# Kernel optimization log

Hardware: AMD Instinct MI355X
Metric: run time of the kernel (lower is better)

The kernel has to match this reference:

```python
import jax, jax.numpy as jnp
import numpy as np


def setup_inputs() -> dict:
    key = jax.random.key(0)
    k1, k2, k3, k4 = jax.random.split(key, 4)
    B, C_in, KH, KW, C_out = 256, 512, 7, 7, 1000
    inputR = jax.random.normal(k1, (B, C_in, KH, KW), dtype=jnp.float32)
    inputSPD = jax.random.normal(k2, (B, C_in, C_in), dtype=jnp.float32)
    fan_in = C_in * KH * KW
    weight = jax.random.normal(k3, (C_out, C_in, KH, KW), dtype=jnp.float32) / np.sqrt(fan_in)
    bias = jax.random.normal(k4, (C_out,), dtype=jnp.float32) / np.sqrt(fan_in)
    return {"inputR": inputR, "inputSPD": inputSPD, "weight": weight, "bias": bias}


def reference(inputR, inputSPD, weight, bias):
    # Conv2d with kernel == spatial size and padding 0 == fully connected layer.
    # outputR: (N, C_out)
    outputR = jnp.einsum('nchw,ochw->no', inputR, weight) + bias

    # top-2 channel selection per sample (indices only; values unused)
    _, top2_idx = jax.lax.top_k(outputR, 2)  # (N, 2)

    # weight is detached for the SPD path in the original module
    w_spd = jax.lax.stop_gradient(weight)[top2_idx]  # (N, 2, C_in, KH, KW)

    # outputSPD[n,k,m] = sum_{c,d,h,w} SPD[n,c,d] * W2[n,k,d,h,w] * W2[n,m,c,h,w]
    # (equivalent to the original's two batched matmuls + sum over (h, w))
    outputSPD = jnp.einsum('ncd,nkdhw,nmchw->nkm', inputSPD, w_spd, w_spd)  # (N, 2, 2)
    return outputR, outputSPD
```

## Files before the change

### kernel.cpp

```cpp
#include <hip/hip_runtime.h>

#define KD 25088
#define N_DIM 1000
#define ZS 28

typedef __attribute__((ext_vector_type(8))) short bf16x8;
typedef __attribute__((ext_vector_type(4))) float f32x4;

__device__ inline unsigned short f2bf(float x) {
  union { float f; unsigned u; } v; v.f = x;
  unsigned r = v.u + 0x7FFFu + ((v.u >> 16) & 1);
  return (unsigned short)(r >> 16);
}
__device__ inline unsigned pack2(float a, float b) {
  return (unsigned)f2bf(a) | ((unsigned)f2bf(b) << 16);
}
__device__ inline float bf2f(unsigned short u) {
  union { unsigned u; float f; } v; v.u = ((unsigned)u) << 16; return v.f;
}

__global__ __launch_bounds__(256) void init_bias_k(
    const float* __restrict__ bias, float* __restrict__ outR) {
  const int id = blockIdx.x * 256 + threadIdx.x;
  if (id < 256 * N_DIM) outR[id] = bias[id % N_DIM];
}

template<int ATOMIC>
__global__ __launch_bounds__(256) void rgemm_k(
    const float* __restrict__ A, const float* __restrict__ W,
    float* __restrict__ D) {
  __shared__ unsigned short As[2][128 * 32];
  __shared__ unsigned short Bs[2][128 * 32];
  const int t = threadIdx.x;
  const int m0 = blockIdx.x * 128;
  const int n0 = blockIdx.y * 128;
  const int z  = blockIdx.z;
  const int lane = t & 63, w = t >> 6;
  const int cw = (w >> 1) * 64, jw = (w & 1) * 64;
  const int r16 = lane & 15, quad = lane >> 4;
  const int srow = t >> 2;
  const int sc8  = (t & 3) << 3;

  float a_pre[16], b_pre[16];

  f32x4 acc[4][4];
#pragma unroll
  for (int i = 0; i < 4; ++i)
#pragma unroll
    for (int j = 0; j < 4; ++j) {
      acc[i][j][0] = 0.f; acc[i][j][1] = 0.f;
      acc[i][j][2] = 0.f; acc[i][j][3] = 0.f;
    }

#define RG_LOAD(s_)                                                         \
  {                                                                         \
    const int kbase = ((z) * ZS + (s_)) * 32;                               \
    _Pragma("unroll")                                                       \
    for (int h = 0; h < 2; ++h) {                                           \
      const int row = h * 64 + srow;                                        \
      const float* pa = A + (size_t)(m0 + row) * KD + kbase + sc8;          \
      *(float4*)&a_pre[h * 8 + 0] = *(const float4*)pa;                     \
      *(float4*)&a_pre[h * 8 + 4] = *(const float4*)(pa + 4);               \
      const int wr = n0 + row;                                              \
      if (wr < N_DIM) {                                                     \
        const float* pw = W + (size_t)wr * KD + kbase + sc8;                \
        *(float4*)&b_pre[h * 8 + 0] = *(const float4*)pw;                   \
        *(float4*)&b_pre[h * 8 + 4] = *(const float4*)(pw + 4);             \
      } else {                                                              \
        _Pragma("unroll")                                                   \
        for (int q = 0; q < 8; ++q) b_pre[h * 8 + q] = 0.f;                 \
      }                                                                     \
    }                                                                       \
  }

#define RG_WRITE(p_)                                                        \
  {                                                                         \
    _Pragma("unroll")                                                       \
    for (int h = 0; h < 2; ++h) {                                           \
      const int row = h * 64 + srow;                                        \
      uint4 ua, ub;                                                         \
      ua.x = pack2(a_pre[h*8+0], a_pre[h*8+1]);                             \
      ua.y = pack2(a_pre[h*8+2], a_pre[h*8+3]);                             \
      ua.z = pack2(a_pre[h*8+4], a_pre[h*8+5]);                             \
      ua.w = pack2(a_pre[h*8+6], a_pre[h*8+7]);                             \
      ub.x = pack2(b_pre[h*8+0], b_pre[h*8+1]);                             \
      ub.y = pack2(b_pre[h*8+2], b_pre[h*8+3]);                             \
      ub.z = pack2(b_pre[h*8+4], b_pre[h*8+5]);                             \
      ub.w = pack2(b_pre[h*8+6], b_pre[h*8+7]);                             \
      *(uint4*)&As[p_][row * 32 + sc8] = ua;                                \
      *(uint4*)&Bs[p_][row * 32 + sc8] = ub;                                \
    }                                                                       \
  }

  RG_LOAD(0); RG_WRITE(0); __syncthreads();
  int p = 0;
  for (int s = 0; s < ZS; ++s) {
    if (s + 1 < ZS) RG_LOAD(s + 1);
    bf16x8 af[4], bq[4];
#pragma unroll
    for (int i = 0; i < 4; ++i) {
      af[i] = *(const bf16x8*)&As[p][(cw + i * 16 + r16) * 32 + quad * 8];
      bq[i] = *(const bf16x8*)&Bs[p][(jw + i * 16 + r16) * 32 + quad * 8];
    }
#pragma unroll
    for (int i = 0; i < 4; ++i)
#pragma unroll
      for (int j = 0; j < 4; ++j)
        acc[i][j] = __builtin_amdgcn_mfma_f32_16x16x32_bf16(af[i], bq[j], acc[i][j], 0, 0, 0);
    if (s + 1 < ZS) RG_WRITE(p ^ 1);
    __syncthreads();
    p ^= 1;
  }

#pragma unroll
  for (int j = 0; j < 4; ++j) {
    const int n = n0 + jw + j * 16 + r16;
    if (n < N_DIM) {
#pragma unroll
      for (int i = 0; i < 4; ++i)
#pragma unroll
        for (int r = 0; r < 4; ++r) {
          const int m = m0 + cw + i * 16 + quad * 4 + r;
          if (ATOMIC)
            atomicAdd(&D[(size_t)m * N_DIM + n], acc[i][j][r]);
          else
            D[((size_t)z * 256 + m) * N_DIM + n] = acc[i][j][r];
        }
    }
  }
#undef RG_LOAD
#undef RG_WRITE
}

template<int FROMPART>
__global__ __launch_bounds__(64) void top8_k(
    const float* __restrict__ src, const float* __restrict__ bias,
    float* __restrict__ outR, int* __restrict__ top2,
    int* __restrict__ candIdx, int* __restrict__ flags,
    float* __restrict__ outSPD) {
  const int n = blockIdx.x;
  const int lane = threadIdx.x;
  float v[16];
  if (FROMPART) {
#pragma unroll
    for (int r = 0; r < 16; ++r) {
      const int o = lane + r * 64;
      v[r] = (o < N_DIM) ? bias[o] : -3.0e38f;
    }
    for (int z = 0; z < ZS; ++z) {
      const float* pz = src + ((size_t)z * 256 + n) * N_DIM;
#pragma unroll
      for (int r = 0; r < 16; ++r) {
        const int o = lane + r * 64;
        if (o < N_DIM) v[r] += pz[o];
      }
    }
#pragma unroll
    for (int r = 0; r < 16; ++r) {
      const int o = lane + r * 64;
      if (o < N_DIM) outR[(size_t)n * N_DIM + o] = v[r];
    }
  } else {
#pragma unroll
    for (int r = 0; r < 16; ++r) {
      const int o = lane + r * 64;
      v[r] = (o < N_DIM) ? src[(size_t)n * N_DIM + o] : -3.0e38f;
    }
  }
  float cv[8]; int ci[8];
#pragma unroll
  for (int rr = 0; rr < 8; ++rr) {
    float bv = -3.0e38f; int bi = 0x3fffffff;
#pragma unroll
    for (int r = 0; r < 16; ++r) {
      const int o = lane + r * 64;
      if (v[r] > bv || (v[r] == bv && o < bi)) { bv = v[r]; bi = o; }
    }
#pragma unroll
    for (int off = 32; off >= 1; off >>= 1) {
      const float ov = __shfl_xor(bv, off, 64);
      const int   oi = __shfl_xor(bi, off, 64);
      if (ov > bv || (ov == bv && oi < bi)) { bv = ov; bi = oi; }
    }
    cv[rr] = bv; ci[rr] = bi;
#pragma unroll
    for (int r = 0; r < 16; ++r)
      if (lane + r * 64 == bi) v[r] = -3.0e38f;
  }
  if (lane == 0) {
    const bool safe = (cv[0] - cv[1] >= 0.025f) &&
                      (cv[1] - cv[2] >= 0.025f) &&
                      (cv[1] - cv[7] >= 0.05f);
    flags[n] = safe ? 0 : 1;
    top2[2 * n]     = ci[0];
    top2[2 * n + 1] = ci[1];
#pragma unroll
    for (int r = 0; r < 8; ++r) candIdx[n * 8 + r] = ci[r];
    outSPD[4 * n + 0] = 0.f; outSPD[4 * n + 1] = 0.f;
    outSPD[4 * n + 2] = 0.f; outSPD[4 * n + 3] = 0.f;
  }
}

__global__ __launch_bounds__(256) void rdot_k(
    const float* __restrict__ A, const float* __restrict__ W,
    const float* __restrict__ bias, const int* __restrict__ candIdx,
    const int* __restrict__ flags, float* __restrict__ vals) {
  const int n = blockIdx.x;
  if (!flags[n]) return;
  const int c = blockIdx.y;
  const int idx = candIdx[n * 8 + c];
  const float4* a4 = (const float4*)(A + (size_t)n * KD);
  const float4* w4 = (const float4*)(W + (size_t)idx * KD);
  float s = 0.f;
  for (int i = threadIdx.x; i < KD / 4; i += 256) {
    const float4 av = a4[i];
    const float4 wv = w4[i];
    s += av.x * wv.x + av.y * wv.y + av.z * wv.z + av.w * wv.w;
  }
#pragma unroll
  for (int off = 32; off >= 1; off >>= 1) s += __shfl_xor(s, off, 64);
  __shared__ float red[4];
  const int lane = threadIdx.x & 63, w = threadIdx.x >> 6;
  if (lane == 0) red[w] = s;
  __syncthreads();
  if (threadIdx.x == 0)
    vals[n * 8 + c] = red[0] + red[1] + red[2] + red[3] + bias[idx];
}

__global__ __launch_bounds__(64) void select_k(
    const float* __restrict__ vals, const int* __restrict__ candIdx,
    const int* __restrict__ flags, int* __restrict__ top2) {
  const int n = blockIdx.x;
  if (threadIdx.x != 0 || !flags[n]) return;
  int b0 = -1; float v0 = -3.0e38f; int i0 = 0x3fffffff;
  for (int c = 0; c < 8; ++c) {
    const int idx = candIdx[n * 8 + c];
    const float vv = vals[n * 8 + c];
    if (vv > v0 || (vv == v0 && idx < i0)) { v0 = vv; i0 = idx; b0 = c; }
  }
  float v1 = -3.0e38f; int i1 = 0x3fffffff;
  for (int c = 0; c < 8; ++c) {
    if (c == b0) continue;
    const int idx = candIdx[n * 8 + c];
    const float vv = vals[n * 8 + c];
    if (vv > v1 || (vv == v1 && idx < i1)) { v1 = vv; i1 = idx; }
  }
  top2[2 * n]     = i0;
  top2[2 * n + 1] = i1;
}

__global__ __launch_bounds__(256) void packsel_k(
    const float* __restrict__ W, const int* __restrict__ candIdx,
    const int* __restrict__ flags, const float* __restrict__ vals,
    unsigned short* __restrict__ Wp) {
  __shared__ unsigned short tile[49 * 130];
  __shared__ int sel_s;
  const int n = blockIdx.x;
  const int which = blockIdx.y;
  const int t = threadIdx.x;
  if (t == 0) {
    int ia, ib;
    if (!flags[n]) {
      ia = candIdx[n * 8];
      ib = candIdx[n * 8 + 1];
    } else {
      int b0 = -1; float v0 = -3.0e38f; int i0 = 0x3fffffff;
      for (int c = 0; c < 8; ++c) {
        const int idx = candIdx[n * 8 + c];
        const float vv = vals[n * 8 + c];
        if (vv > v0 || (vv == v0 && idx < i0)) { v0 = vv; i0 = idx; b0 = c; }
      }
      float v1 = -3.0e38f; int i1 = 0x3fffffff;
      for (int c = 0; c < 8; ++c) {
        if (c == b0) continue;
        const int idx = candIdx[n * 8 + c];
        const float vv = vals[n * 8 + c];
        if (vv > v1 || (vv == v1 && idx < i1)) { v1 = vv; i1 = idx; }
      }
      ia = i0; ib = i1;
    }
    sel_s = which ? ib : ia;
  }
  unsigned short* dstn = Wp + (size_t)n * 65536;
  {
    const int r0 = 98 + which * 15;
    for (int u = t; u < 15 * 128; u += 256) {
      const int rr = u >> 7;
      const int cc = (u & 127) << 1;
      *(unsigned*)(dstn + (size_t)(r0 + rr) * 512 + cc) = 0u;
    }
  }
  __syncthreads();
  const int sel = sel_s;
  const float4* src4 = (const float4*)(W + (size_t)sel * KD);
  for (int chunk = 0; chunk < 4; ++chunk) {
    const float4* s4 = src4 + chunk * 1568;
    for (int u4 = t; u4 < 1568; u4 += 256) {
      const float4 fv = s4[u4];
      const float vv[4] = {fv.x, fv.y, fv.z, fv.w};
      const int i0 = u4 * 4;
#pragma unroll
      for (int e = 0; e < 4; ++e) {
        const int idx = i0 + e;
        const int c = idx / 49;
        const int hw = idx - c * 49;
        tile[hw * 130 + c] = f2bf(vv[e]);
      }
    }
    __syncthreads();
    const int cp = t & 63, hwb = t >> 6;
    unsigned short* wbase = dstn + (size_t)which * 49 * 512 + chunk * 128 + 2 * cp;
#pragma unroll
    for (int it = 0; it < 13; ++it) {
      const int hw = hwb + it * 4;
      if (hw < 49) {
        const unsigned val = *(const unsigned*)&tile[hw * 130 + 2 * cp];
        *(unsigned*)(wbase + (size_t)hw * 512) = val;
      }
    }
    __syncthreads();
  }
}

__global__ __launch_bounds__(256) void spd_k(
    const float* __restrict__ S, const unsigned short* __restrict__ Wp,
    float* __restrict__ outSPD) {
  __shared__ unsigned short As[2][128 * 32];
  __shared__ unsigned short Bs[2][128 * 32];
  __shared__ float red[4];
  const int t = threadIdx.x;
  const int n  = blockIdx.x >> 2;
  const int c0 = (blockIdx.x & 3) * 128;
  const float* Sn = S + (size_t)n * 512 * 512;
  const unsigned short* Wpn = Wp + (size_t)n * 65536;
  const int lane = t & 63, w = t >> 6;
  const int cw = (w >> 1) * 64, jw = (w & 1) * 64;
  const int r16 = lane & 15, quad = lane >> 4;
  const int srow = t >> 2;
  const int sc8  = (t & 3) << 3;

  if (t < 4) red[t] = 0.f;

  float a_pre[16];
  uint4 b_pre[2];

  f32x4 acc[4][4];
#pragma unroll
  for (int i = 0; i < 4; ++i)
#pragma unroll
    for (int j = 0; j < 4; ++j) {
      acc[i][j][0] = 0.f; acc[i][j][1] = 0.f;
      acc[i][j][2] = 0.f; acc[i][j][3] = 0.f;
    }

#define SP_LOAD(s_)                                                         \
  {                                                                         \
    const int d0 = (s_) * 32;                                               \
    _Pragma("unroll")                                                       \
    for (int h = 0; h < 2; ++h) {                                           \
      const int row = h * 64 + srow;                                        \
      const float* pa = Sn + (size_t)(c0 + row) * 512 + d0 + sc8;           \
      *(float4*)&a_pre[h * 8 + 0] = *(const float4*)pa;                     \
      *(float4*)&a_pre[h * 8 + 4] = *(const float4*)(pa + 4);               \
      b_pre[h] = *(const uint4*)(Wpn + (size_t)row * 512 + d0 + sc8);       \
    }                                                                       \
  }

#define SP_WRITE(p_)                                                        \
  {                                                                         \
    _Pragma("unroll")                                                       \
    for (int h = 0; h < 2; ++h) {                                           \
      const int row = h * 64 + srow;                                        \
      uint4 ua;                                                             \
      ua.x = pack2(a_pre[h*8+0], a_pre[h*8+1]);                             \
      ua.y = pack2(a_pre[h*8+2], a_pre[h*8+3]);                             \
      ua.z = pack2(a_pre[h*8+4], a_pre[h*8+5]);                             \
      ua.w = pack2(a_pre[h*8+6], a_pre[h*8+7]);                             \
      *(uint4*)&As[p_][row * 32 + sc8] = ua;                                \
      *(uint4*)&Bs[p_][row * 32 + sc8] = b_pre[h];                          \
    }                                                                       \
  }

  SP_LOAD(0); SP_WRITE(0); __syncthreads();
  int p = 0;
  for (int s = 0; s < 16; ++s) {
    if (s + 1 < 16) SP_LOAD(s + 1);
    bf16x8 af[4], bq[4];
#pragma unroll
    for (int i = 0; i < 4; ++i) {
      af[i] = *(const bf16x8*)&As[p][(cw + i * 16 + r16) * 32 + quad * 8];
      bq[i] = *(const bf16x8*)&Bs[p][(jw + i * 16 + r16) * 32 + quad * 8];
    }
#pragma unroll
    for (int i = 0; i < 4; ++i)
#pragma unroll
      for (int j = 0; j < 4; ++j)
        acc[i][j] = __builtin_amdgcn_mfma_f32_16x16x32_bf16(af[i], bq[j], acc[i][j], 0, 0, 0);
    if (s + 1 < 16) SP_WRITE(p ^ 1);
    __syncthreads();
    p ^= 1;
  }
#undef SP_LOAD
#undef SP_WRITE

  float p00 = 0.f, p01 = 0.f, p10 = 0.f, p11 = 0.f;
#pragma unroll
  for (int j = 0; j < 4; ++j) {
    const int jj = jw + j * 16 + r16;
    if (jj < 98) {
      const int kk = (jj >= 49);
      const int hw = jj - 49 * kk;
      const unsigned short* wa = Wpn + (size_t)hw * 512;
      const unsigned short* wb = Wpn + (size_t)(49 + hw) * 512;
#pragma unroll
      for (int i = 0; i < 4; ++i) {
#pragma unroll
        for (int r = 0; r < 4; ++r) {
          const int c = c0 + cw + i * 16 + quad * 4 + r;
          const float u   = acc[i][j][r];
          const float wav = bf2f(wa[c]);
          const float wbv = bf2f(wb[c]);
          if (kk == 0) { p00 = fmaf(u, wav, p00); p01 = fmaf(u, wbv, p01); }
          else         { p10 = fmaf(u, wav, p10); p11 = fmaf(u, wbv, p11); }
        }
      }
    }
  }

  atomicAdd(&red[0], p00);
  atomicAdd(&red[1], p01);
  atomicAdd(&red[2], p10);
  atomicAdd(&red[3], p11);
  __syncthreads();
  if (t < 4) atomicAdd(&outSPD[n * 4 + t], red[t]);
}

__global__ __launch_bounds__(256) void spd_fb_k(
    const float* __restrict__ S, const float* __restrict__ W,
    const int* __restrict__ top2, float* __restrict__ outSPD) {
  __shared__ unsigned short As[128 * 40];
  __shared__ unsigned short Bs[128 * 40];
  __shared__ float red[4];
  const int t = threadIdx.x;
  const int n  = blockIdx.x >> 2;
  const int c0 = (blockIdx.x & 3) * 128;
  const int ia = top2[2 * n];
  const int ib = top2[2 * n + 1];
  const float* Sn = S + (size_t)n * 512 * 512;
  const int lane = t & 63, w = t >> 6;
  const int cw = (w >> 1) * 64, jw = (w & 1) * 64;
  const int r16 = lane & 15, quad = lane >> 4;
  if (t < 4) red[t] = 0.f;
  f32x4 acc[4][4];
#pragma unroll
  for (int i = 0; i < 4; ++i)
#pragma unroll
    for (int j = 0; j < 4; ++j) {
      acc[i][j][0] = 0.f; acc[i][j][1] = 0.f;
      acc[i][j][2] = 0.f; acc[i][j][3] = 0.f;
    }
  const int bj  = t & 127;
  const int bh  = t >> 7;
  const int bkk = (bj >= 49);
  const int bhw = bj - 49 * bkk;
  const bool bvalid = (bj < 98);
  const float* brow = W + (size_t)(bkk ? ib : ia) * KD + bhw;
  for (int d0 = 0; d0 < 512; d0 += 32) {
#pragma unroll
    for (int h = 0; h < 4; ++h) {
      const int idx = h * 256 + t;
      const int row = idx >> 3;
      const int c4  = (idx & 7) << 2;
      float4 av = *(const float4*)(Sn + (size_t)(c0 + row) * 512 + d0 + c4);
      uint2 pa;
      pa.x = pack2(av.x, av.y);
      pa.y = pack2(av.z, av.w);
      *(uint2*)&As[row * 40 + c4] = pa;
    }
#pragma unroll
    for (int dd2 = 0; dd2 < 16; dd2 += 2) {
      const int dd = bh * 16 + dd2;
      const float x0 = bvalid ? brow[(size_t)(d0 + dd) * 49] : 0.f;
      const float x1 = bvalid ? brow[(size_t)(d0 + dd + 1) * 49] : 0.f;
      *(unsigned*)&Bs[bj * 40 + dd] = pack2(x0, x1);
    }
    __syncthreads();
    bf16x8 af[4], bq[4];
#pragma unroll
    for (int i = 0; i < 4; ++i) {
      af[i] = *(const bf16x8*)&As[(cw + i * 16 + r16) * 40 + quad * 8];
      bq[i] = *(const bf16x8*)&Bs[(jw + i * 16 + r16) * 40 + quad * 8];
    }
#pragma unroll
    for (int i = 0; i < 4; ++i)
#pragma unroll
      for (int j = 0; j < 4; ++j)
        acc[i][j] = __builtin_amdgcn_mfma_f32_16x16x32_bf16(af[i], bq[j], acc[i][j], 0, 0, 0);
    __syncthreads();
  }
  float p00 = 0.f, p01 = 0.f, p10 = 0.f, p11 = 0.f;
  const float* Wa = W + (size_t)ia * KD;
  const float* Wb = W + (size_t)ib * KD;
#pragma unroll
  for (int j = 0; j < 4; ++j) {
    const int jj = jw + j * 16 + r16;
    if (jj < 98) {
      const int kk = (jj >= 49);
      const int hw = jj - 49 * kk;
#pragma unroll
      for (int i = 0; i < 4; ++i)
#pragma unroll
        for (int r = 0; r < 4; ++r) {
          const int c = c0 + cw + i * 16 + quad * 4 + r;
          const float u  = acc[i][j][r];
          const float wa = Wa[(size_t)c * 49 + hw];
          const float wb = Wb[(size_t)c * 49 + hw];
          if (kk == 0) { p00 = fmaf(u, wa, p00); p01 = fmaf(u, wb, p01); }
          else         { p10 = fmaf(u, wa, p10); p11 = fmaf(u, wb, p11); }
        }
    }
  }
  atomicAdd(&red[0], p00);
  atomicAdd(&red[1], p01);
  atomicAdd(&red[2], p10);
  atomicAdd(&red[3], p11);
  __syncthreads();
  if (t < 4) atomicAdd(&outSPD[n * 4 + t], red[t]);
}

extern "C" void kernel_launch(void* const* d_in, const int* in_sizes, int n_in,
                              void* d_out, int out_size, void* d_ws, size_t ws_size,
                              hipStream_t stream) {
  const float* inputR   = (const float*)d_in[0];
  const float* inputSPD = (const float*)d_in[1];
  const float* weight   = (const float*)d_in[2];
  const float* bias     = (const float*)d_in[3];
  float* out = (float*)d_out;

  int*   top2    = (int*)d_ws;
  int*   candIdx = (int*)((char*)d_ws + 2048);
  int*   flags   = (int*)((char*)d_ws + 2048 + 8192);
  float* vals    = (float*)((char*)d_ws + 2048 + 8192 + 1024);
  float* part    = (float*)((char*)d_ws + 65536);
  const size_t PART_BYTES = (size_t)ZS * 256 * N_DIM * 4;
  unsigned short* Wp = (unsigned short*)((char*)d_ws + 65536 + PART_BYTES);
  const bool bigws = ws_size >= 65536ull + PART_BYTES + 256ull * 65536ull * 2ull;

  if (bigws) {
    rgemm_k<0><<<dim3(2, 8, ZS), 256, 0, stream>>>(inputR, weight, part);
    top8_k<1><<<dim3(256), 64, 0, stream>>>(part, bias, out, top2, candIdx, flags, out + 256000);
    rdot_k<<<dim3(256, 8), 256, 0, stream>>>(inputR, weight, bias, candIdx, flags, vals);
    packsel_k<<<dim3(256, 2), 256, 0, stream>>>(weight, candIdx, flags, vals, Wp);
    spd_k<<<dim3(1024), 256, 0, stream>>>(inputSPD, Wp, out + 256000);
  } else {
    init_bias_k<<<dim3(1000), 256, 0, stream>>>(bias, out);
    rgemm_k<1><<<dim3(2, 8, ZS), 256, 0, stream>>>(inputR, weight, out);
    top8_k<0><<<dim3(256), 64, 0, stream>>>(out, bias, out, top2, candIdx, flags, out + 256000);
    rdot_k<<<dim3(256, 8), 256, 0, stream>>>(inputR, weight, bias, candIdx, flags, vals);
    select_k<<<dim3(256), 64, 0, stream>>>(vals, candIdx, flags, top2);
    spd_fb_k<<<dim3(1024), 256, 0, stream>>>(inputSPD, weight, top2, out + 256000);
  }
}
```

Before: 635.1 us.

## Use hardware bf16 pack, remap block IDs across XCDs, skip padded MFMA tiles

Replaces the software round-to-nearest bf16 conversion with the v_cvt_pk_bf16_f32 instruction. Both GEMM kernels move to a flattened 1D grid whose block-id decoding spreads neighbouring tiles across the 8 XCDs, which is meant to improve L2 locality. MFMA issues and LDS reads for the last 16-column sub-tile are skipped where those columns are padding (N beyond 1000 in rgemm, jj beyond 98 in spd). The mapping assumes exactly 448 and 1024 blocks, and the hardware conversion's rounding may differ slightly from the old code on edge values.

```diff
diff --git a/kernel.cpp b/kernel.cpp
--- a/kernel.cpp
+++ b/kernel.cpp
@@ -7,13 +7,15 @@
 typedef __attribute__((ext_vector_type(8))) short bf16x8;
 typedef __attribute__((ext_vector_type(4))) float f32x4;
 
+__device__ inline unsigned pack2(float a, float b) {
+  unsigned r;
+  asm("v_cvt_pk_bf16_f32 %0, %1, %2" : "=v"(r) : "v"(a), "v"(b));
+  return r;
+}
 __device__ inline unsigned short f2bf(float x) {
-  union { float f; unsigned u; } v; v.f = x;
-  unsigned r = v.u + 0x7FFFu + ((v.u >> 16) & 1);
-  return (unsigned short)(r >> 16);
-}
-__device__ inline unsigned pack2(float a, float b) {
-  return (unsigned)f2bf(a) | ((unsigned)f2bf(b) << 16);
+  unsigned r;
+  asm("v_cvt_pk_bf16_f32 %0, %1, %1" : "=v"(r) : "v"(x));
+  return (unsigned short)r;
 }
 __device__ inline float bf2f(unsigned short u) {
   union { unsigned u; float f; } v; v.u = ((unsigned)u) << 16; return v.f;
@@ -32,14 +34,17 @@
   __shared__ unsigned short As[2][128 * 32];
   __shared__ unsigned short Bs[2][128 * 32];
   const int t = threadIdx.x;
-  const int m0 = blockIdx.x * 128;
-  const int n0 = blockIdx.y * 128;
-  const int z  = blockIdx.z;
+  const int id  = blockIdx.x;
+  const int mz  = (id & 7) * 7 + ((id >> 3) >> 3);
+  const int n0  = ((id >> 3) & 7) * 128;
+  const int m0  = (mz / ZS) * 128;
+  const int z   = mz % ZS;
   const int lane = t & 63, w = t >> 6;
   const int cw = (w >> 1) * 64, jw = (w & 1) * 64;
   const int r16 = lane & 15, quad = lane >> 4;
   const int srow = t >> 2;
   const int sc8  = (t & 3) << 3;
+  const bool doj3 = (n0 + jw + 48) < N_DIM;
 
   float a_pre[16], b_pre[16];
 
@@ -100,13 +105,15 @@
 #pragma unroll
     for (int i = 0; i < 4; ++i) {
       af[i] = *(const bf16x8*)&As[p][(cw + i * 16 + r16) * 32 + quad * 8];
-      bq[i] = *(const bf16x8*)&Bs[p][(jw + i * 16 + r16) * 32 + quad * 8];
+      if (i < 3 || doj3)
+        bq[i] = *(const bf16x8*)&Bs[p][(jw + i * 16 + r16) * 32 + quad * 8];
     }
 #pragma unroll
     for (int i = 0; i < 4; ++i)
 #pragma unroll
       for (int j = 0; j < 4; ++j)
-        acc[i][j] = __builtin_amdgcn_mfma_f32_16x16x32_bf16(af[i], bq[j], acc[i][j], 0, 0, 0);
+        if (j < 3 || doj3)
+          acc[i][j] = __builtin_amdgcn_mfma_f32_16x16x32_bf16(af[i], bq[j], acc[i][j], 0, 0, 0);
     if (s + 1 < ZS) RG_WRITE(p ^ 1);
     __syncthreads();
     p ^= 1;
@@ -329,8 +336,9 @@
   __shared__ unsigned short Bs[2][128 * 32];
   __shared__ float red[4];
   const int t = threadIdx.x;
-  const int n  = blockIdx.x >> 2;
-  const int c0 = (blockIdx.x & 3) * 128;
+  const int id = blockIdx.x;
+  const int n  = (id & 7) * 32 + ((id >> 3) >> 2);
+  const int c0 = ((id >> 3) & 3) * 128;
   const float* Sn = S + (size_t)n * 512 * 512;
   const unsigned short* Wpn = Wp + (size_t)n * 65536;
   const int lane = t & 63, w = t >> 6;
@@ -338,6 +346,7 @@
   const int r16 = lane & 15, quad = lane >> 4;
   const int srow = t >> 2;
   const int sc8  = (t & 3) << 3;
+  const bool doj3 = (jw == 0);
 
   if (t < 4) red[t] = 0.f;
 
@@ -389,13 +398,15 @@
 #pragma unroll
     for (int i = 0; i < 4; ++i) {
       af[i] = *(const bf16x8*)&As[p][(cw + i * 16 + r16) * 32 + quad * 8];
-      bq[i] = *(const bf16x8*)&Bs[p][(jw + i * 16 + r16) * 32 + quad * 8];
+      if (i < 3 || doj3)
+        bq[i] = *(const bf16x8*)&Bs[p][(jw + i * 16 + r16) * 32 + quad * 8];
     }
 #pragma unroll
     for (int i = 0; i < 4; ++i)
 #pragma unroll
       for (int j = 0; j < 4; ++j)
-        acc[i][j] = __builtin_amdgcn_mfma_f32_16x16x32_bf16(af[i], bq[j], acc[i][j], 0, 0, 0);
+        if (j < 3 || doj3)
+          acc[i][j] = __builtin_amdgcn_mfma_f32_16x16x32_bf16(af[i], bq[j], acc[i][j], 0, 0, 0);
     if (s + 1 < 16) SP_WRITE(p ^ 1);
     __syncthreads();
     p ^= 1;
@@ -547,14 +558,14 @@
   const bool bigws = ws_size >= 65536ull + PART_BYTES + 256ull * 65536ull * 2ull;
 
   if (bigws) {
-    rgemm_k<0><<<dim3(2, 8, ZS), 256, 0, stream>>>(inputR, weight, part);
+    rgemm_k<0><<<dim3(448), 256, 0, stream>>>(inputR, weight, part);
     top8_k<1><<<dim3(256), 64, 0, stream>>>(part, bias, out, top2, candIdx, flags, out + 256000);
     rdot_k<<<dim3(256, 8), 256, 0, stream>>>(inputR, weight, bias, candIdx, flags, vals);
     packsel_k<<<dim3(256, 2), 256, 0, stream>>>(weight, candIdx, flags, vals, Wp);
     spd_k<<<dim3(1024), 256, 0, stream>>>(inputSPD, Wp, out + 256000);
   } else {
     init_bias_k<<<dim3(1000), 256, 0, stream>>>(bias, out);
-    rgemm_k<1><<<dim3(2, 8, ZS), 256, 0, stream>>>(inputR, weight, out);
+    rgemm_k<1><<<dim3(448), 256, 0, stream>>>(inputR, weight, out);
     top8_k<0><<<dim3(256), 64, 0, stream>>>(out, bias, out, top2, candIdx, flags, out + 256000);
     rdot_k<<<dim3(256, 8), 256, 0, stream>>>(inputR, weight, bias, candIdx, flags, vals);
     select_k<<<dim3(256), 64, 0, stream>>>(vals, candIdx, flags, top2);
```

Measured after the change: 627.5 us. About the same (-1.2%).
